# Kernel optimization log

Hardware: AMD Instinct MI355X
Metric: run time of the kernel (lower is better)

The kernel has to match this reference:

```python
import jax, jax.numpy as jnp
import numpy as np

N = 20000      # nodes
E = 200000     # edges
IN = 128       # in_feat
OUT = 128      # out_feat
NB = 8         # num_bases
SI = IN // NB  # submat_in = 16
SO = OUT // NB # submat_out = 16
R = 230        # num_rels
T = 365        # total_times


def setup_inputs() -> dict:
    key = jax.random.key(0)
    ks = jax.random.split(key, 11)
    h = jax.random.normal(ks[0], (N, IN), jnp.float32)
    edge_norm = jax.random.uniform(ks[1], (E, 1), jnp.float32)
    node_norm = jax.random.uniform(ks[2], (N, 1), jnp.float32)
    weight = jax.random.normal(ks[3], (R, NB * SI * SO), jnp.float32) * 0.05
    h_bias = jnp.zeros((OUT,), jnp.float32)
    loop_weight = jax.random.normal(ks[4], (IN, OUT), jnp.float32) * 0.05
    time_embed = jax.random.normal(ks[5], (T, IN), jnp.float32) * 0.05
    edge_src = jax.random.randint(ks[6], (E,), 0, N)
    edge_dst = jax.random.randint(ks[7], (E,), 0, N)
    edge_type = jax.random.randint(ks[8], (E,), 0, R)
    time_idx = jax.random.randint(ks[9], (N,), 0, T)
    return dict(h=h, edge_norm=edge_norm, node_norm=node_norm, weight=weight,
                h_bias=h_bias, loop_weight=loop_weight, time_embed=time_embed,
                edge_src=edge_src, edge_dst=edge_dst, edge_type=edge_type,
                time_idx=time_idx)


def reference(h, edge_norm, node_norm, weight, h_bias, loop_weight, time_embed,
              edge_src, edge_dst, edge_type, time_idx):
    # self-loop message
    loop_message = h @ loop_weight                              # [N, OUT]
    # msg_func: per-edge relation weight gather + block-diagonal bmm
    W_e = weight[edge_type].reshape(-1, NB, SI, SO)             # [E, NB, SI, SO]
    src = h[edge_src].reshape(-1, NB, SI)                       # [E, NB, SI]
    msg = jnp.einsum('ebi,ebio->ebo', src, W_e).reshape(-1, OUT)  # [E, OUT]
    msg = msg * edge_norm
    # fn.sum aggregation over destination nodes
    agg = jax.ops.segment_sum(msg, edge_dst, num_segments=N)    # [N, OUT]
    # apply_func: scale by node norm, then bias + self loop + activation
    node_repr = agg * node_norm
    node_repr = node_repr + h_bias + loop_message
    node_repr = jax.nn.relu(node_repr)
    # get_time_embedding: per-node time embedding gather
    time_embedding = time_embed[time_idx]                       # [N, IN]
    return node_repr, time_embedding
```

## Files before the change

kernel.cpp:

```cpp
#include <hip/hip_runtime.h>

#define N 20000
#define E 200000
#define IN 128
#define OUT 128
#define NB 8
#define SI 16
#define SO 16
#define R 230
#define T 365

__device__ float g_W_t[(size_t)R * NB * SO * SI];
__device__ float g_msg[(size_t)E * OUT];
__device__ int   g_cnt_d[N];
__device__ int   g_off_d[N];
__device__ int   g_cur_d[N];
__device__ int   g_cnt_r[R * 16];
__device__ int   g_cur_r[R * 16];
__device__ int   g_pos[E];
__device__ int   g_eid_r[E];
__device__ int   g_total_d;
__device__ int   g_total_r;

__global__ void init_kernel(const float* __restrict__ weight) {
    int t = blockIdx.x * blockDim.x + threadIdx.x;
    if (t < R * NB * SO * SI) {
        int r  = t >> 11;
        int b  = (t >> 8) & 7;
        int ol = (t >> 4) & 15;
        int i  = t & 15;
        g_W_t[t] = weight[(long)r * 2048 + b * 256 + i * 16 + ol];
    }
    if (t < N) g_cnt_d[t] = 0;
    if (t < R * 16) g_cnt_r[t] = 0;
    if (t == 0) { g_total_d = 0; g_total_r = 0; }
}

__global__ __launch_bounds__(256) void hist_kernel(
        const int* __restrict__ edge_dst,
        const int* __restrict__ edge_type) {
    __shared__ int lh[R];
    for (int j = threadIdx.x; j < R; j += 256) lh[j] = 0;
    __syncthreads();
    for (long e = (long)blockIdx.x * blockDim.x + threadIdx.x; e < E;
         e += (long)gridDim.x * blockDim.x) {
        atomicAdd(&g_cnt_d[edge_dst[e]], 1);
        atomicAdd(&lh[edge_type[e]], 1);
    }
    __syncthreads();
    for (int j = threadIdx.x; j < R; j += 256)
        if (lh[j]) atomicAdd(&g_cnt_r[j * 16], lh[j]);
}

__global__ __launch_bounds__(256) void alloc_kernel() {
    int idx  = blockIdx.x * blockDim.x + threadIdx.x;
    int lane = threadIdx.x & 63;
    const int NPAD = 20032;
    if (idx < NPAD) {
        int c = (idx < N) ? g_cnt_d[idx] : 0;
        int x = c;
        for (int d = 1; d < 64; d <<= 1) {
            int y = __shfl_up(x, d);
            if (lane >= d) x += y;
        }
        int base = 0;
        if (lane == 63) base = atomicAdd(&g_total_d, x);
        base = __shfl(base, 63);
        if (idx < N) {
            int off = base + x - c;
            g_off_d[idx] = off;
            g_cur_d[idx] = off;
        }
    } else if (idx < NPAD + 256) {
        int j = idx - NPAD;
        int c = (j < R) ? g_cnt_r[j * 16] : 0;
        int x = c;
        for (int d = 1; d < 64; d <<= 1) {
            int y = __shfl_up(x, d);
            if (lane >= d) x += y;
        }
        int base = 0;
        if (lane == 63) base = atomicAdd(&g_total_r, x);
        base = __shfl(base, 63);
        if (j < R) g_cur_r[j * 16] = base + x - c;
    }
}

__global__ void scatter_kernel(const int* __restrict__ edge_dst,
                               const int* __restrict__ edge_type) {
    int e = blockIdx.x * blockDim.x + threadIdx.x;
    if (e < E) {
        g_pos[e] = atomicAdd(&g_cur_d[edge_dst[e]], 1);
        int pr = atomicAdd(&g_cur_r[edge_type[e] * 16], 1);
        g_eid_r[pr] = e;
    }
}

__global__ __launch_bounds__(256) void msg_kernel(
        const float* __restrict__ h,
        const float* __restrict__ edge_norm,
        const int* __restrict__ edge_src,
        const int* __restrict__ edge_type) {
    __shared__ __attribute__((aligned(16))) float hsm[64 * 132];
    __shared__ int   ssrc[64], stype[64], spos[64];
    __shared__ float snorm[64];

    const int tid = threadIdx.x;
    const int lo  = blockIdx.x * 64;

    if (tid < 64) {
        int e = g_eid_r[lo + tid];
        ssrc[tid]  = edge_src[e];
        stype[tid] = edge_type[e];
        snorm[tid] = edge_norm[e];
        spos[tid]  = g_pos[e];
    }
    __syncthreads();

    {
        const int row = tid >> 2;
        const int c0  = (tid & 3) * 4;
        const float* hp = h + (long)ssrc[row] * IN;
        float* dst = &hsm[row * 132];
#pragma unroll
        for (int j = 0; j < 8; ++j) {
            float4 v = *reinterpret_cast<const float4*>(hp + c0 + 16 * j);
            *reinterpret_cast<float4*>(dst + c0 + 16 * j) = v;
        }
    }
    __syncthreads();

    const int slot = tid >> 7;
    const int o    = tid & 127;
    const int b    = o >> 4;
    const int ol   = o & 15;

#define MSG_BODY(K, W0, W1, W2, W3)                                          \
    {                                                                        \
        const float* hrow = &hsm[(K) * 132 + b * 16];                        \
        float4 h0 = *reinterpret_cast<const float4*>(hrow);                  \
        float4 h1 = *reinterpret_cast<const float4*>(hrow + 4);              \
        float4 h2 = *reinterpret_cast<const float4*>(hrow + 8);              \
        float4 h3 = *reinterpret_cast<const float4*>(hrow + 12);             \
        float m0 = 0.f, m1 = 0.f;                                            \
        m0 = fmaf(h0.x, W0.x, m0); m0 = fmaf(h0.y, W0.y, m0);                \
        m0 = fmaf(h0.z, W0.z, m0); m0 = fmaf(h0.w, W0.w, m0);                \
        m1 = fmaf(h1.x, W1.x, m1); m1 = fmaf(h1.y, W1.y, m1);                \
        m1 = fmaf(h1.z, W1.z, m1); m1 = fmaf(h1.w, W1.w, m1);                \
        m0 = fmaf(h2.x, W2.x, m0); m0 = fmaf(h2.y, W2.y, m0);                \
        m0 = fmaf(h2.z, W2.z, m0); m0 = fmaf(h2.w, W2.w, m0);                \
        m1 = fmaf(h3.x, W3.x, m1); m1 = fmaf(h3.y, W3.y, m1);                \
        m1 = fmaf(h3.z, W3.z, m1); m1 = fmaf(h3.w, W3.w, m1);                \
        g_msg[(long)spos[K] * OUT + o] = snorm[K] * (m0 + m1);               \
    }

    if (stype[0] == stype[63]) {
        const float4* wp = reinterpret_cast<const float4*>(
            g_W_t + (long)stype[0] * 2048 + b * 256 + ol * 16);
        float4 w0 = wp[0], w1 = wp[1], w2 = wp[2], w3 = wp[3];
#pragma unroll 4
        for (int k = slot; k < 64; k += 2)
            MSG_BODY(k, w0, w1, w2, w3)
    } else {
        int rcur = -1;
        float4 w0, w1, w2, w3;
        for (int k = slot; k < 64; k += 2) {
            int r = stype[k];
            if (r != rcur) {
                const float4* wp = reinterpret_cast<const float4*>(
                    g_W_t + (long)r * 2048 + b * 256 + ol * 16);
                w0 = wp[0]; w1 = wp[1]; w2 = wp[2]; w3 = wp[3];
                rcur = r;
            }
            MSG_BODY(k, w0, w1, w2, w3)
        }
    }
#undef MSG_BODY
}

__global__ __launch_bounds__(128) void node_kernel(
        const float* __restrict__ h,
        const float* __restrict__ node_norm,
        const float* __restrict__ h_bias,
        const float* __restrict__ loop_weight,
        const float* __restrict__ time_embed,
        const int* __restrict__ time_idx,
        float* __restrict__ out) {
    __shared__ float hsm[IN * 8];
    const int o    = threadIdx.x;
    const int base = blockIdx.x * 8;

    for (int k = o; k < 8 * IN; k += 128) {
        int nl = k >> 7;
        int i  = k & 127;
        hsm[i * 8 + nl] = h[(long)(base + nl) * IN + i];
    }
    __syncthreads();

    float acc[8];
#pragma unroll
    for (int nl = 0; nl < 8; ++nl) {
        int n  = base + nl;
        int st = g_off_d[n];
        int cn = g_cnt_d[n];
        float a0 = 0.f, a1 = 0.f, a2 = 0.f, a3 = 0.f;
        const float* mp = g_msg + (long)st * OUT + o;
        int k = 0;
        for (; k + 3 < cn; k += 4) {
            a0 += mp[(long)(k + 0) * OUT];
            a1 += mp[(long)(k + 1) * OUT];
            a2 += mp[(long)(k + 2) * OUT];
            a3 += mp[(long)(k + 3) * OUT];
        }
        for (; k < cn; ++k) a0 += mp[(long)k * OUT];
        acc[nl] = ((a0 + a1) + (a2 + a3)) * node_norm[n];
    }

    float sl[8];
#pragma unroll
    for (int nl = 0; nl < 8; ++nl) sl[nl] = 0.f;

    for (int i0 = 0; i0 < IN; i0 += 8) {
        float w[8];
#pragma unroll
        for (int j = 0; j < 8; ++j)
            w[j] = loop_weight[(long)(i0 + j) * OUT + o];
#pragma unroll
        for (int j = 0; j < 8; ++j) {
            const float* row = &hsm[(i0 + j) * 8];
            float4 p0 = *reinterpret_cast<const float4*>(row);
            float4 p1 = *reinterpret_cast<const float4*>(row + 4);
            sl[0] = fmaf(p0.x, w[j], sl[0]); sl[1] = fmaf(p0.y, w[j], sl[1]);
            sl[2] = fmaf(p0.z, w[j], sl[2]); sl[3] = fmaf(p0.w, w[j], sl[3]);
            sl[4] = fmaf(p1.x, w[j], sl[4]); sl[5] = fmaf(p1.y, w[j], sl[5]);
            sl[6] = fmaf(p1.z, w[j], sl[6]); sl[7] = fmaf(p1.w, w[j], sl[7]);
        }
    }

    const float bias = h_bias[o];
#pragma unroll
    for (int nl = 0; nl < 8; ++nl) {
        int n = base + nl;
        float v = acc[nl] + bias + sl[nl];
        out[(long)n * OUT + o] = fmaxf(v, 0.f);
        out[(long)N * OUT + (long)n * IN + o] =
            time_embed[(long)time_idx[n] * IN + o];
    }
}

extern "C" void kernel_launch(void* const* d_in, const int* in_sizes, int n_in,
                              void* d_out, int out_size, void* d_ws, size_t ws_size,
                              hipStream_t stream) {
    const float* h           = (const float*)d_in[0];
    const float* edge_norm   = (const float*)d_in[1];
    const float* node_norm   = (const float*)d_in[2];
    const float* weight      = (const float*)d_in[3];
    const float* h_bias      = (const float*)d_in[4];
    const float* loop_weight = (const float*)d_in[5];
    const float* time_embed  = (const float*)d_in[6];
    const int*   edge_src    = (const int*)d_in[7];
    const int*   edge_dst    = (const int*)d_in[8];
    const int*   edge_type   = (const int*)d_in[9];
    const int*   time_idx    = (const int*)d_in[10];
    float* out = (float*)d_out;

    init_kernel<<<(R * NB * SO * SI + 255) / 256, 256, 0, stream>>>(weight);
    hist_kernel<<<400, 256, 0, stream>>>(edge_dst, edge_type);
    alloc_kernel<<<(20032 + 256 + 255) / 256, 256, 0, stream>>>();
    scatter_kernel<<<(E + 255) / 256, 256, 0, stream>>>(edge_dst, edge_type);
    msg_kernel<<<E / 64, 256, 0, stream>>>(h, edge_norm, edge_src, edge_type);
    node_kernel<<<N / 8, 128, 0, stream>>>(h, node_norm, h_bias, loop_weight,
                                           time_embed, time_idx, out);
}
```

Measured before the change: 227.9 us.

## Store edge messages as bf16, fold init into hist, reset counters in node kernel

```diff
diff --git a/kernel.cpp b/kernel.cpp
--- a/kernel.cpp
+++ b/kernel.cpp
@@ -10,45 +10,48 @@
 #define R 230
 #define T 365
 
-__device__ float g_W_t[(size_t)R * NB * SO * SI];
-__device__ float g_msg[(size_t)E * OUT];
-__device__ int   g_cnt_d[N];
-__device__ int   g_off_d[N];
-__device__ int   g_cur_d[N];
-__device__ int   g_cnt_r[R * 16];
-__device__ int   g_cur_r[R * 16];
-__device__ int   g_pos[E];
-__device__ int   g_eid_r[E];
-__device__ int   g_total_d;
-__device__ int   g_total_r;
-
-__global__ void init_kernel(const float* __restrict__ weight) {
-    int t = blockIdx.x * blockDim.x + threadIdx.x;
-    if (t < R * NB * SO * SI) {
+__device__ float  g_W_t[(size_t)R * NB * SO * SI];
+__device__ ushort g_msg[(size_t)E * OUT];
+__device__ int    g_cnt_d[N];
+__device__ int    g_off_d[N];
+__device__ int    g_cur_d[N];
+__device__ int    g_cnt_r[R * 16];
+__device__ int    g_cur_r[R * 16];
+__device__ int    g_pos[E];
+__device__ int    g_eid_r[E];
+__device__ int    g_total_d;
+__device__ int    g_total_r;
+
+__device__ __forceinline__ ushort f2bf(float f) {
+    unsigned u = __float_as_uint(f);
+    return (ushort)((u + 0x7fffu + ((u >> 16) & 1u)) >> 16);
+}
+__device__ __forceinline__ float bf2f(ushort v) {
+    return __uint_as_float((unsigned)v << 16);
+}
+
+__global__ __launch_bounds__(256) void hist_kernel(
+        const float* __restrict__ weight,
+        const int* __restrict__ edge_dst,
+        const int* __restrict__ edge_type) {
+    __shared__ int lh[R];
+    const int tid  = threadIdx.x;
+    const int gtid = blockIdx.x * 256 + tid;
+    for (int t = gtid; t < R * NB * SI * SO; t += gridDim.x * 256) {
         int r  = t >> 11;
         int b  = (t >> 8) & 7;
         int ol = (t >> 4) & 15;
         int i  = t & 15;
         g_W_t[t] = weight[(long)r * 2048 + b * 256 + i * 16 + ol];
     }
-    if (t < N) g_cnt_d[t] = 0;
-    if (t < R * 16) g_cnt_r[t] = 0;
-    if (t == 0) { g_total_d = 0; g_total_r = 0; }
-}
-
-__global__ __launch_bounds__(256) void hist_kernel(
-        const int* __restrict__ edge_dst,
-        const int* __restrict__ edge_type) {
-    __shared__ int lh[R];
-    for (int j = threadIdx.x; j < R; j += 256) lh[j] = 0;
-    __syncthreads();
-    for (long e = (long)blockIdx.x * blockDim.x + threadIdx.x; e < E;
-         e += (long)gridDim.x * blockDim.x) {
+    for (int j = tid; j < R; j += 256) lh[j] = 0;
+    __syncthreads();
+    for (long e = gtid; e < E; e += (long)gridDim.x * 256) {
         atomicAdd(&g_cnt_d[edge_dst[e]], 1);
         atomicAdd(&lh[edge_type[e]], 1);
     }
     __syncthreads();
-    for (int j = threadIdx.x; j < R; j += 256)
+    for (int j = tid; j < R; j += 256)
         if (lh[j]) atomicAdd(&g_cnt_r[j * 16], lh[j]);
 }
 
@@ -101,14 +104,14 @@
         const float* __restrict__ edge_norm,
         const int* __restrict__ edge_src,
         const int* __restrict__ edge_type) {
-    __shared__ __attribute__((aligned(16))) float hsm[64 * 132];
-    __shared__ int   ssrc[64], stype[64], spos[64];
-    __shared__ float snorm[64];
+    __shared__ __attribute__((aligned(16))) float hsm[32 * 132];
+    __shared__ int   ssrc[32], stype[32], spos[32];
+    __shared__ float snorm[32];
 
     const int tid = threadIdx.x;
-    const int lo  = blockIdx.x * 64;
-
-    if (tid < 64) {
+    const int lo  = blockIdx.x * 32;
+
+    if (tid < 32) {
         int e = g_eid_r[lo + tid];
         ssrc[tid]  = edge_src[e];
         stype[tid] = edge_type[e];
@@ -118,14 +121,14 @@
     __syncthreads();
 
     {
-        const int row = tid >> 2;
-        const int c0  = (tid & 3) * 4;
+        const int row = tid >> 3;
+        const int c0  = (tid & 7) * 4;
         const float* hp = h + (long)ssrc[row] * IN;
         float* dst = &hsm[row * 132];
 #pragma unroll
-        for (int j = 0; j < 8; ++j) {
-            float4 v = *reinterpret_cast<const float4*>(hp + c0 + 16 * j);
-            *reinterpret_cast<float4*>(dst + c0 + 16 * j) = v;
+        for (int j = 0; j < 4; ++j) {
+            float4 v = *reinterpret_cast<const float4*>(hp + c0 + 32 * j);
+            *reinterpret_cast<float4*>(dst + c0 + 32 * j) = v;
         }
     }
     __syncthreads();
@@ -151,20 +154,21 @@
         m0 = fmaf(h2.z, W2.z, m0); m0 = fmaf(h2.w, W2.w, m0);                \
         m1 = fmaf(h3.x, W3.x, m1); m1 = fmaf(h3.y, W3.y, m1);                \
         m1 = fmaf(h3.z, W3.z, m1); m1 = fmaf(h3.w, W3.w, m1);                \
-        g_msg[(long)spos[K] * OUT + o] = snorm[K] * (m0 + m1);               \
-    }
-
-    if (stype[0] == stype[63]) {
+        __builtin_nontemporal_store(f2bf(snorm[K] * (m0 + m1)),              \
+                                    &g_msg[(long)spos[K] * OUT + o]);        \
+    }
+
+    if (stype[0] == stype[31]) {
         const float4* wp = reinterpret_cast<const float4*>(
             g_W_t + (long)stype[0] * 2048 + b * 256 + ol * 16);
         float4 w0 = wp[0], w1 = wp[1], w2 = wp[2], w3 = wp[3];
 #pragma unroll 4
-        for (int k = slot; k < 64; k += 2)
+        for (int k = slot; k < 32; k += 2)
             MSG_BODY(k, w0, w1, w2, w3)
     } else {
         int rcur = -1;
         float4 w0, w1, w2, w3;
-        for (int k = slot; k < 64; k += 2) {
+        for (int k = slot; k < 32; k += 2) {
             int r = stype[k];
             if (r != rcur) {
                 const float4* wp = reinterpret_cast<const float4*>(
@@ -204,15 +208,16 @@
         int st = g_off_d[n];
         int cn = g_cnt_d[n];
         float a0 = 0.f, a1 = 0.f, a2 = 0.f, a3 = 0.f;
-        const float* mp = g_msg + (long)st * OUT + o;
+        const ushort* mp = g_msg + (long)st * OUT + o;
         int k = 0;
         for (; k + 3 < cn; k += 4) {
-            a0 += mp[(long)(k + 0) * OUT];
-            a1 += mp[(long)(k + 1) * OUT];
-            a2 += mp[(long)(k + 2) * OUT];
-            a3 += mp[(long)(k + 3) * OUT];
-        }
-        for (; k < cn; ++k) a0 += mp[(long)k * OUT];
+            a0 += bf2f(__builtin_nontemporal_load(&mp[(long)(k + 0) * OUT]));
+            a1 += bf2f(__builtin_nontemporal_load(&mp[(long)(k + 1) * OUT]));
+            a2 += bf2f(__builtin_nontemporal_load(&mp[(long)(k + 2) * OUT]));
+            a3 += bf2f(__builtin_nontemporal_load(&mp[(long)(k + 3) * OUT]));
+        }
+        for (; k < cn; ++k)
+            a0 += bf2f(__builtin_nontemporal_load(&mp[(long)k * OUT]));
         acc[nl] = ((a0 + a1) + (a2 + a3)) * node_norm[n];
     }
 
@@ -246,6 +251,14 @@
         out[(long)N * OUT + (long)n * IN + o] =
             time_embed[(long)time_idx[n] * IN + o];
     }
+
+    __syncthreads();
+    if (o < 8) g_cnt_d[base + o] = 0;
+    {
+        int j = blockIdx.x * 128 + o;
+        if (j < R * 16) g_cnt_r[j] = 0;
+    }
+    if (blockIdx.x == 0 && o == 0) { g_total_d = 0; g_total_r = 0; }
 }
 
 extern "C" void kernel_launch(void* const* d_in, const int* in_sizes, int n_in,
@@ -264,11 +277,10 @@
     const int*   time_idx    = (const int*)d_in[10];
     float* out = (float*)d_out;
 
-    init_kernel<<<(R * NB * SO * SI + 255) / 256, 256, 0, stream>>>(weight);
-    hist_kernel<<<400, 256, 0, stream>>>(edge_dst, edge_type);
-    alloc_kernel<<<(20032 + 256 + 255) / 256, 256, 0, stream>>>();
+    hist_kernel<<<400, 256, 0, stream>>>(weight, edge_dst, edge_type);
+    alloc_kernel<<<80, 256, 0, stream>>>();
     scatter_kernel<<<(E + 255) / 256, 256, 0, stream>>>(edge_dst, edge_type);
-    msg_kernel<<<E / 64, 256, 0, stream>>>(h, edge_norm, edge_src, edge_type);
+    msg_kernel<<<E / 32, 256, 0, stream>>>(h, edge_norm, edge_src, edge_type);
     node_kernel<<<N / 8, 128, 0, stream>>>(h, node_norm, h_bias, loop_weight,
                                            time_embed, time_idx, out);
 }
```

After: 229.5 us. Within noise of the previous version (+0.7%).
